# Kernel tuning notes

Measured on AMD Instinct MI355X. Metric: run time of the kernel, lower is better.

## Reference

```python
import jax, jax.numpy as jnp
import numpy as np

N_NODES = 100000
N_EDGES = 1600000
IN_F, HID_F, N_CLS = 512, 128, 64


def spmm(row, col, val, x, n):
    # out[i] = sum_{e: row[e]==i} val[e] * x[col[e]]  (sparse adj @ x)
    msgs = val[:, None] * x[col]          # [E, F] gather + scale
    return jax.ops.segment_sum(msgs, row, num_segments=n)


def setup_inputs() -> dict:
    key = jax.random.key(0)
    k = jax.random.split(key, 8)
    x = jax.random.normal(k[0], (N_NODES, IN_F), dtype=jnp.float32)
    adj_row = jax.random.randint(k[1], (N_EDGES,), 0, N_NODES, dtype=jnp.int32)
    adj_col = jax.random.randint(k[2], (N_EDGES,), 0, N_NODES, dtype=jnp.int32)
    adj_val = jax.random.uniform(k[3], (N_EDGES,), dtype=jnp.float32)
    s1 = 1.0 / np.sqrt(IN_F)
    s2 = 1.0 / np.sqrt(HID_F)
    w1 = jax.random.uniform(k[4], (IN_F, HID_F), jnp.float32, -s1, s1)
    b1 = jax.random.uniform(k[5], (HID_F,), jnp.float32, -s1, s1)
    w2 = jax.random.uniform(k[6], (HID_F, N_CLS), jnp.float32, -s2, s2)
    b2 = jax.random.uniform(k[7], (N_CLS,), jnp.float32, -s2, s2)
    return {"x": x, "adj_row": adj_row, "adj_col": adj_col, "adj_val": adj_val,
            "w1": w1, "b1": b1, "w2": w2, "b2": b2}


def reference(x, adj_row, adj_col, adj_val, w1, b1, w2, b2):
    n = x.shape[0]
    # conv1: dense projection then sparse aggregation
    h = spmm(adj_row, adj_col, adj_val, x @ w1 + b1, n)
    h = jax.nn.relu(h)  # dropout is identity in eval mode
    # conv2
    out = spmm(adj_row, adj_col, adj_val, h @ w2 + b2, n)
    return out
```

## Files before the change

### kernel.cpp

```cpp
#include <hip/hip_runtime.h>
#include <hip/hip_bf16.h>


constexpr int N_NODES = 100000;
constexpr int IN_F    = 512;
constexpr int HID_F   = 128;
constexpr int N_CLS   = 64;
constexpr int N_EDGES = 1600000;

constexpr int SCAN_BLOCK    = 256;
constexpr int N_SCAN_BLOCKS = (N_NODES + SCAN_BLOCK - 1) / SCAN_BLOCK;
constexpr int NB_GEMM       = (N_NODES + 255) / 256;

typedef __attribute__((ext_vector_type(8))) short short8;
typedef __attribute__((ext_vector_type(4))) float f32x4;

static __device__ __forceinline__ unsigned short f2bf(float x) {
    unsigned int u = __float_as_uint(x);
    unsigned int r = (u + 0x7FFFu + ((u >> 16) & 1u)) >> 16;
    return (unsigned short)r;
}
static __device__ __forceinline__ float bf2f(unsigned short u) {
    return __uint_as_float(((unsigned int)u) << 16);
}

__global__ void w1t_kernel(const float* __restrict__ w1, unsigned short* __restrict__ w1t)
{
    int idx = blockIdx.x * 256 + threadIdx.x;
    int n = idx >> 9, k = idx & 511;
    w1t[idx] = f2bf(w1[k * HID_F + n]);
}

__global__ void w2t_kernel(const float* __restrict__ w2, unsigned short* __restrict__ w2t)
{
    int idx = blockIdx.x * 256 + threadIdx.x;
    int n = idx >> 7, k = idx & 127;
    w2t[idx] = f2bf(w2[k * N_CLS + n]);
}

__global__ void zero_int_kernel(int* __restrict__ p, int n)
{
    int i = blockIdx.x * blockDim.x + threadIdx.x;
    if (i < n) p[i] = 0;
}

__global__ void hist_kernel(const int* __restrict__ row, int* __restrict__ counts)
{
    int e = blockIdx.x * blockDim.x + threadIdx.x;
    if (e < N_EDGES) atomicAdd(&counts[row[e]], 1);
}

__global__ __launch_bounds__(SCAN_BLOCK) void scanA_kernel(
    const int* __restrict__ counts, int* __restrict__ local_ex,
    int* __restrict__ blockSums)
{
    __shared__ int s[SCAN_BLOCK];
    const int t = threadIdx.x;
    const int i = blockIdx.x * SCAN_BLOCK + t;
    int v = (i < N_NODES) ? counts[i] : 0;
    s[t] = v;
    __syncthreads();
    for (int off = 1; off < SCAN_BLOCK; off <<= 1) {
        int u = (t >= off) ? s[t - off] : 0;
        __syncthreads();
        s[t] += u;
        __syncthreads();
    }
    if (i < N_NODES) local_ex[i] = s[t] - v;
    if (t == SCAN_BLOCK - 1) blockSums[blockIdx.x] = s[t];
}

__global__ __launch_bounds__(512) void scanB_kernel(int* __restrict__ blockSums)
{
    __shared__ int s[512];
    const int t = threadIdx.x;
    int v = (t < N_SCAN_BLOCKS) ? blockSums[t] : 0;
    s[t] = v;
    __syncthreads();
    for (int off = 1; off < 512; off <<= 1) {
        int u = (t >= off) ? s[t - off] : 0;
        __syncthreads();
        s[t] += u;
        __syncthreads();
    }
    if (t < N_SCAN_BLOCKS) blockSums[t] = s[t] - v;
}

__global__ __launch_bounds__(SCAN_BLOCK) void scanC_kernel(
    const int* __restrict__ local_ex, const int* __restrict__ blockSums,
    int* __restrict__ row_ptr, int* __restrict__ cursor)
{
    const int i = blockIdx.x * SCAN_BLOCK + threadIdx.x;
    if (i < N_NODES) {
        int v = local_ex[i] + blockSums[blockIdx.x];
        row_ptr[i] = v;
        cursor[i]  = v;
    }
    if (i == 0) row_ptr[N_NODES] = N_EDGES;
}

__global__ void scatter_kernel(
    const int* __restrict__ row, const int* __restrict__ col,
    const float* __restrict__ val, int* __restrict__ cursor,
    int2* __restrict__ es)
{
    int e = blockIdx.x * blockDim.x + threadIdx.x;
    if (e < N_EDGES) {
        int pos = atomicAdd(&cursor[row[e]], 1);
        es[pos] = make_int2(col[e], __float_as_int(val[e]));
    }
}

__global__ __launch_bounds__(512, 4) void gemm1_mfma_kernel(
    const float* __restrict__ x, const unsigned short* __restrict__ w1t,
    const float* __restrict__ b1, unsigned short* __restrict__ h0b)
{
    __shared__ unsigned short Bs[128 * 256];
    char* lb = (char*)Bs;

    const int tid  = threadIdx.x;
    const int lane = tid & 63;
    const int w    = tid >> 6;
    const int m = lane & 15;
    const int q = lane >> 4;
    const int row0 = blockIdx.x * 256 + w * 32;
    const bool active = row0 < N_NODES;

    f32x4 acc[2][8];
#pragma unroll
    for (int mi = 0; mi < 2; ++mi)
#pragma unroll
        for (int ni = 0; ni < 8; ++ni)
            acc[mi][ni] = (f32x4){0.f, 0.f, 0.f, 0.f};

    union U8 { short8 v; __hip_bfloat162 h[4]; };

    const float* a0p = x + (size_t)(row0 + m)      * IN_F + q * 8;
    const float* a1p = x + (size_t)(row0 + 16 + m) * IN_F + q * 8;
    const int swz = (m & 7) << 4;

    for (int p = 0; p < 2; ++p) {
        {
            const unsigned short* src = w1t + p * 256;
#pragma unroll
            for (int i = 0; i < 8; ++i) {
                int chunk = tid + i * 512;
                int n   = chunk >> 5;
                int k16 = chunk & 31;
                short8 v = *(const short8*)(src + (size_t)n * IN_F + k16 * 8);
                *(short8*)(lb + ((n * 512 + k16 * 16) ^ ((n & 7) << 4))) = v;
            }
        }
        __syncthreads();

        if (active) {
            const float* a0 = a0p + p * 256;
            const float* a1 = a1p + p * 256;
            float4 c0l = ((const float4*)a0)[0];
            float4 c0h = ((const float4*)a0)[1];
            float4 c1l = ((const float4*)a1)[0];
            float4 c1h = ((const float4*)a1)[1];

#pragma unroll
            for (int t = 0; t < 8; ++t) {
                float4 n0l, n0h, n1l, n1h;
                if (t + 1 < 8) {
                    n0l = ((const float4*)(a0 + (t + 1) * 32))[0];
                    n0h = ((const float4*)(a0 + (t + 1) * 32))[1];
                    n1l = ((const float4*)(a1 + (t + 1) * 32))[0];
                    n1h = ((const float4*)(a1 + (t + 1) * 32))[1];
                }

                U8 u0, u1;
                u0.h[0] = __float22bfloat162_rn(make_float2(c0l.x, c0l.y));
                u0.h[1] = __float22bfloat162_rn(make_float2(c0l.z, c0l.w));
                u0.h[2] = __float22bfloat162_rn(make_float2(c0h.x, c0h.y));
                u0.h[3] = __float22bfloat162_rn(make_float2(c0h.z, c0h.w));
                u1.h[0] = __float22bfloat162_rn(make_float2(c1l.x, c1l.y));
                u1.h[1] = __float22bfloat162_rn(make_float2(c1l.z, c1l.w));
                u1.h[2] = __float22bfloat162_rn(make_float2(c1h.x, c1h.y));
                u1.h[3] = __float22bfloat162_rn(make_float2(c1h.z, c1h.w));
                short8 av0 = u0.v, av1 = u1.v;

                const int kb = t * 64 + q * 16;
#pragma unroll
                for (int ni = 0; ni < 8; ++ni) {
                    int off = (((ni * 16 + m) * 512) + kb) ^ swz;
                    short8 bfr = *(const short8*)(lb + off);
                    acc[0][ni] = __builtin_amdgcn_mfma_f32_16x16x32_bf16(av0, bfr, acc[0][ni], 0, 0, 0);
                    acc[1][ni] = __builtin_amdgcn_mfma_f32_16x16x32_bf16(av1, bfr, acc[1][ni], 0, 0, 0);
                }

                c0l = n0l; c0h = n0h; c1l = n1l; c1h = n1h;
            }
        }
        __syncthreads();
    }

    if (!active) return;

    float bias[8];
#pragma unroll
    for (int ni = 0; ni < 8; ++ni) bias[ni] = b1[ni * 16 + m];

#pragma unroll
    for (int mi = 0; mi < 2; ++mi)
#pragma unroll
        for (int r = 0; r < 4; ++r) {
            int row = row0 + mi * 16 + q * 4 + r;
            unsigned short* dst = h0b + (size_t)row * HID_F;
#pragma unroll
            for (int ni = 0; ni < 8; ++ni)
                dst[ni * 16 + m] = f2bf(acc[mi][ni][r] + bias[ni]);
        }
}

__global__ __launch_bounds__(512, 4) void gemm2_mfma_kernel(
    const unsigned short* __restrict__ h1r, const unsigned short* __restrict__ w2t,
    const float* __restrict__ b2, float* __restrict__ h2)
{
    __shared__ unsigned short Bs[64 * 128];
    char* lb = (char*)Bs;

    const int tid  = threadIdx.x;
    const int lane = tid & 63;
    const int w    = tid >> 6;
    const int m = lane & 15;
    const int q = lane >> 4;
    const int row0 = blockIdx.x * 256 + w * 32;
    const bool active = row0 < N_NODES;

#pragma unroll
    for (int i = 0; i < 2; ++i) {
        int chunk = tid + i * 512;
        int n   = chunk >> 4;
        int k16 = chunk & 15;
        short8 v = *(const short8*)(w2t + (size_t)n * HID_F + k16 * 8);
        *(short8*)(lb + ((n * 256 + k16 * 16) ^ ((n & 7) << 4))) = v;
    }
    __syncthreads();
    if (!active) return;

    const unsigned short* a0p = h1r + (size_t)(row0 + m)      * HID_F + q * 8;
    const unsigned short* a1p = h1r + (size_t)(row0 + 16 + m) * HID_F + q * 8;

    short8 a0[4], a1[4];
#pragma unroll
    for (int t = 0; t < 4; ++t) {
        a0[t] = *(const short8*)(a0p + t * 32);
        a1[t] = *(const short8*)(a1p + t * 32);
    }

    f32x4 acc[2][4];
#pragma unroll
    for (int mi = 0; mi < 2; ++mi)
#pragma unroll
        for (int ni = 0; ni < 4; ++ni)
            acc[mi][ni] = (f32x4){0.f, 0.f, 0.f, 0.f};

    const int swz = (m & 7) << 4;
#pragma unroll
    for (int t = 0; t < 4; ++t) {
        const int kb = t * 64 + q * 16;
#pragma unroll
        for (int ni = 0; ni < 4; ++ni) {
            int off = (((ni * 16 + m) * 256) + kb) ^ swz;
            short8 b = *(const short8*)(lb + off);
            acc[0][ni] = __builtin_amdgcn_mfma_f32_16x16x32_bf16(a0[t], b, acc[0][ni], 0, 0, 0);
            acc[1][ni] = __builtin_amdgcn_mfma_f32_16x16x32_bf16(a1[t], b, acc[1][ni], 0, 0, 0);
        }
    }

    float bias[4];
#pragma unroll
    for (int ni = 0; ni < 4; ++ni) bias[ni] = b2[ni * 16 + m];

#pragma unroll
    for (int mi = 0; mi < 2; ++mi)
#pragma unroll
        for (int r = 0; r < 4; ++r) {
            int row = row0 + mi * 16 + q * 4 + r;
            float* dst = h2 + (size_t)row * N_CLS;
#pragma unroll
            for (int ni = 0; ni < 4; ++ni)
                dst[ni * 16 + m] = acc[mi][ni][r] + bias[ni];
        }
}

__global__ __launch_bounds__(256) void spmm_g128_kernel(
    const int* __restrict__ rp, const int2* __restrict__ es,
    const unsigned short* __restrict__ src, unsigned short* __restrict__ dst)
{
    const int r = blockIdx.x * 4 + threadIdx.y;
    if (r >= N_NODES) return;
    const int lane = threadIdx.x;
    const int j0 = rp[r], j1 = rp[r + 1];

    float ax = 0.f, ay = 0.f;
    int j = j0;
    for (; j + 7 < j1; j += 8) {
        int2 e[8];
        ushort2 u[8];
#pragma unroll
        for (int t = 0; t < 8; ++t) e[t] = es[j + t];
#pragma unroll
        for (int t = 0; t < 8; ++t)
            u[t] = ((const ushort2*)(src + (size_t)e[t].x * HID_F))[lane];
#pragma unroll
        for (int t = 0; t < 8; ++t) {
            float v = __int_as_float(e[t].y);
            ax += v * bf2f(u[t].x);
            ay += v * bf2f(u[t].y);
        }
    }
    if (j + 3 < j1) {
        int2 e[4];
        ushort2 u[4];
#pragma unroll
        for (int t = 0; t < 4; ++t) e[t] = es[j + t];
#pragma unroll
        for (int t = 0; t < 4; ++t)
            u[t] = ((const ushort2*)(src + (size_t)e[t].x * HID_F))[lane];
#pragma unroll
        for (int t = 0; t < 4; ++t) {
            float v = __int_as_float(e[t].y);
            ax += v * bf2f(u[t].x);
            ay += v * bf2f(u[t].y);
        }
        j += 4;
    }
    for (; j < j1; ++j) {
        int2 e = es[j];
        float v = __int_as_float(e.y);
        ushort2 u = ((const ushort2*)(src + (size_t)e.x * HID_F))[lane];
        ax += v * bf2f(u.x);
        ay += v * bf2f(u.y);
    }
    ushort2 o;
    o.x = f2bf(fmaxf(ax, 0.f));
    o.y = f2bf(fmaxf(ay, 0.f));
    ((ushort2*)(dst + (size_t)r * HID_F))[lane] = o;
}

__global__ __launch_bounds__(256) void spmm_g64_kernel(
    const int* __restrict__ rp, const int2* __restrict__ es,
    const float* __restrict__ src, float* __restrict__ dst)
{
    const int r = blockIdx.x * 4 + threadIdx.y;
    if (r >= N_NODES) return;
    const int lane = threadIdx.x;
    const int j0 = rp[r], j1 = rp[r + 1];

    float acc = 0.f;
    int j = j0;
    for (; j + 7 < j1; j += 8) {
        int2 e[8];
        float a[8];
#pragma unroll
        for (int t = 0; t < 8; ++t) e[t] = es[j + t];
#pragma unroll
        for (int t = 0; t < 8; ++t)
            a[t] = src[(size_t)e[t].x * N_CLS + lane];
#pragma unroll
        for (int t = 0; t < 8; ++t)
            acc += __int_as_float(e[t].y) * a[t];
    }
    if (j + 3 < j1) {
        int2 e[4];
        float a[4];
#pragma unroll
        for (int t = 0; t < 4; ++t) e[t] = es[j + t];
#pragma unroll
        for (int t = 0; t < 4; ++t)
            a[t] = src[(size_t)e[t].x * N_CLS + lane];
#pragma unroll
        for (int t = 0; t < 4; ++t)
            acc += __int_as_float(e[t].y) * a[t];
        j += 4;
    }
    for (; j < j1; ++j) {
        int2 e = es[j];
        acc += __int_as_float(e.y) * src[(size_t)e.x * N_CLS + lane];
    }
    dst[(size_t)r * N_CLS + lane] = acc;
}

extern "C" void kernel_launch(void* const* d_in, const int* in_sizes, int n_in,
                              void* d_out, int out_size, void* d_ws, size_t ws_size,
                              hipStream_t stream)
{
    const float* x       = (const float*)d_in[0];
    const int*   adj_row = (const int*)  d_in[1];
    const int*   adj_col = (const int*)  d_in[2];
    const float* adj_val = (const float*)d_in[3];
    const float* w1      = (const float*)d_in[4];
    const float* b1      = (const float*)d_in[5];
    const float* w2      = (const float*)d_in[6];
    const float* b2      = (const float*)d_in[7];
    float*       out     = (float*)d_out;

    char* ws = (char*)d_ws;
    unsigned short* h0b   = (unsigned short*)ws;
    unsigned short* h1r   = (unsigned short*)(ws + 25600000);
    float*          h2    = (float*)(ws + 51200000);
    int2*           es    = (int2*) (ws + 76800000);
    int*            rp    = (int*)  (ws + 89600000);
    int*            cur   = (int*)  (ws + 90000016);
    unsigned short* w1t   = (unsigned short*)(ws + 90400016);
    int*            lex   = (int*)  (ws + 90531088);
    int*            bsum  = (int*)  (ws + 90931088);
    unsigned short* w2t   = (unsigned short*)(ws + 90932656);

    w1t_kernel<<<IN_F * HID_F / 256, 256, 0, stream>>>(w1, w1t);
    w2t_kernel<<<HID_F * N_CLS / 256, 256, 0, stream>>>(w2, w2t);
    zero_int_kernel<<<(N_NODES + 255) / 256, 256, 0, stream>>>(cur, N_NODES);
    hist_kernel<<<(N_EDGES + 255) / 256, 256, 0, stream>>>(adj_row, cur);
    scanA_kernel<<<N_SCAN_BLOCKS, SCAN_BLOCK, 0, stream>>>(cur, lex, bsum);
    scanB_kernel<<<1, 512, 0, stream>>>(bsum);
    scanC_kernel<<<N_SCAN_BLOCKS, SCAN_BLOCK, 0, stream>>>(lex, bsum, rp, cur);
    scatter_kernel<<<(N_EDGES + 255) / 256, 256, 0, stream>>>(
        adj_row, adj_col, adj_val, cur, es);

    gemm1_mfma_kernel<<<NB_GEMM, 512, 0, stream>>>(x, w1t, b1, h0b);
    spmm_g128_kernel<<<(N_NODES + 3) / 4, dim3(64, 4), 0, stream>>>(
        rp, es, h0b, h1r);

    gemm2_mfma_kernel<<<NB_GEMM, 512, 0, stream>>>(h1r, w2t, b2, h2);
    spmm_g64_kernel<<<(N_NODES + 3) / 4, dim3(64, 4), 0, stream>>>(
        rp, es, h2, out);
}
```

Before: 660.1 us.

## Fuse GEMM1 with edge scatter and merge weight-prep and histogram kernels

The weight transpose, weight conversion and edge histogram kernels are merged into one prep kernel, and the zeroing kernel becomes a memset. GEMM1 is retiled to 64 rows per 256-thread block and interleaved with the CSR scatter in a single launch, with even blocks doing GEMM and odd blocks doing scatter. The aim is to overlap the atomic-bound scatter with the bandwidth-bound GEMM and to cut launch count. GEMM output is now staged through LDS so rows are written to global memory with coalesced 16-byte stores. The cost is reloading W1 tiles more often per row and mixing very different workloads in one grid.

```diff
diff --git a/kernel.cpp b/kernel.cpp
--- a/kernel.cpp
+++ b/kernel.cpp
@@ -10,7 +10,11 @@
 
 constexpr int SCAN_BLOCK    = 256;
 constexpr int N_SCAN_BLOCKS = (N_NODES + SCAN_BLOCK - 1) / SCAN_BLOCK;
-constexpr int NB_GEMM       = (N_NODES + 255) / 256;
+constexpr int NB_GEMM2      = (N_NODES + 255) / 256;
+
+constexpr int NB_G1 = (N_NODES + 63) / 64;
+constexpr int NB_SC = (N_EDGES + 1023) / 1024;
+constexpr int NB_FUSED = NB_G1 + NB_SC;
 
 typedef __attribute__((ext_vector_type(8))) short short8;
 typedef __attribute__((ext_vector_type(4))) float f32x4;
@@ -24,30 +28,25 @@
     return __uint_as_float(((unsigned int)u) << 16);
 }
 
-__global__ void w1t_kernel(const float* __restrict__ w1, unsigned short* __restrict__ w1t)
-{
-    int idx = blockIdx.x * 256 + threadIdx.x;
-    int n = idx >> 9, k = idx & 511;
-    w1t[idx] = f2bf(w1[k * HID_F + n]);
-}
-
-__global__ void w2t_kernel(const float* __restrict__ w2, unsigned short* __restrict__ w2t)
-{
-    int idx = blockIdx.x * 256 + threadIdx.x;
-    int n = idx >> 7, k = idx & 127;
-    w2t[idx] = f2bf(w2[k * N_CLS + n]);
-}
-
-__global__ void zero_int_kernel(int* __restrict__ p, int n)
-{
-    int i = blockIdx.x * blockDim.x + threadIdx.x;
-    if (i < n) p[i] = 0;
-}
-
-__global__ void hist_kernel(const int* __restrict__ row, int* __restrict__ counts)
-{
-    int e = blockIdx.x * blockDim.x + threadIdx.x;
-    if (e < N_EDGES) atomicAdd(&counts[row[e]], 1);
+__global__ __launch_bounds__(256) void prep_kernel(
+    const float* __restrict__ w1, const float* __restrict__ w2,
+    const int* __restrict__ row,
+    unsigned short* __restrict__ w1t, unsigned short* __restrict__ w2t,
+    int* __restrict__ counts)
+{
+    const int bid = blockIdx.x;
+    if (bid < 256) {
+        int idx = bid * 256 + threadIdx.x;
+        int n = idx >> 9, k = idx & 511;
+        w1t[idx] = f2bf(w1[k * HID_F + n]);
+    } else if (bid < 288) {
+        int idx = (bid - 256) * 256 + threadIdx.x;
+        int n = idx >> 7, k = idx & 127;
+        w2t[idx] = f2bf(w2[k * N_CLS + n]);
+    } else {
+        int e = (bid - 288) * 256 + threadIdx.x;
+        if (e < N_EDGES) atomicAdd(&counts[row[e]], 1);
+    }
 }
 
 __global__ __launch_bounds__(SCAN_BLOCK) void scanA_kernel(
@@ -99,23 +98,127 @@
     if (i == 0) row_ptr[N_NODES] = N_EDGES;
 }
 
-__global__ void scatter_kernel(
+__global__ __launch_bounds__(256, 4) void fused_g1_scatter_kernel(
+    const float* __restrict__ x, const unsigned short* __restrict__ w1t,
+    const float* __restrict__ b1, unsigned short* __restrict__ h0b,
     const int* __restrict__ row, const int* __restrict__ col,
     const float* __restrict__ val, int* __restrict__ cursor,
     int2* __restrict__ es)
 {
-    int e = blockIdx.x * blockDim.x + threadIdx.x;
-    if (e < N_EDGES) {
-        int pos = atomicAdd(&cursor[row[e]], 1);
-        es[pos] = make_int2(col[e], __float_as_int(val[e]));
-    }
-}
-
-__global__ __launch_bounds__(512, 4) void gemm1_mfma_kernel(
-    const float* __restrict__ x, const unsigned short* __restrict__ w1t,
-    const float* __restrict__ b1, unsigned short* __restrict__ h0b)
-{
-    __shared__ unsigned short Bs[128 * 256];
+    __shared__ unsigned short Bs[128 * 128];
+    char* lb = (char*)Bs;
+    const int tid = threadIdx.x;
+    const int bid = blockIdx.x;
+
+    if (bid & 1) {
+        const int base = (bid >> 1) * 1024 + tid;
+#pragma unroll
+        for (int i = 0; i < 4; ++i) {
+            int e = base + i * 256;
+            if (e < N_EDGES) {
+                int r = row[e];
+                int pos = atomicAdd(&cursor[r], 1);
+                es[pos] = make_int2(col[e], __float_as_int(val[e]));
+            }
+        }
+        return;
+    }
+
+    const int gid  = bid >> 1;
+    const int lane = tid & 63;
+    const int w    = tid >> 6;
+    const int m = lane & 15;
+    const int q = lane >> 4;
+    const int row0 = gid * 64;
+    const int myrow = row0 + w * 16 + m;
+    const int arow  = (myrow < N_NODES) ? myrow : (N_NODES - 1);
+
+    f32x4 acc[8];
+#pragma unroll
+    for (int ni = 0; ni < 8; ++ni)
+        acc[ni] = (f32x4){0.f, 0.f, 0.f, 0.f};
+
+    union U8 { short8 v; __hip_bfloat162 h[4]; };
+
+    const float* ap = x + (size_t)arow * IN_F + q * 8;
+    const int swz = (m & 7) << 4;
+
+    float4 a0l = ((const float4*)ap)[0];
+    float4 a0h = ((const float4*)ap)[1];
+    float4 a1l = ((const float4*)(ap + 32))[0];
+    float4 a1h = ((const float4*)(ap + 32))[1];
+
+#pragma unroll
+    for (int t = 0; t < 16; ++t) {
+        if ((t & 3) == 0) {
+            if (t) __syncthreads();
+            const unsigned short* src = w1t + (t >> 2) * 128;
+#pragma unroll
+            for (int i = 0; i < 8; ++i) {
+                int c = tid + i * 256;
+                int n = c >> 4, k16 = c & 15;
+                short8 v = *(const short8*)(src + (size_t)n * IN_F + k16 * 8);
+                *(short8*)(lb + ((n * 256 + k16 * 16) ^ ((n & 7) << 4))) = v;
+            }
+            __syncthreads();
+        }
+
+        float4 nl, nh;
+        if (t + 2 < 16) {
+            nl = ((const float4*)(ap + (t + 2) * 32))[0];
+            nh = ((const float4*)(ap + (t + 2) * 32))[1];
+        }
+
+        U8 u;
+        u.h[0] = __float22bfloat162_rn(make_float2(a0l.x, a0l.y));
+        u.h[1] = __float22bfloat162_rn(make_float2(a0l.z, a0l.w));
+        u.h[2] = __float22bfloat162_rn(make_float2(a0h.x, a0h.y));
+        u.h[3] = __float22bfloat162_rn(make_float2(a0h.z, a0h.w));
+        short8 av = u.v;
+
+        const int kb = (t & 3) * 64 + q * 16;
+#pragma unroll
+        for (int ni = 0; ni < 8; ++ni) {
+            int off = (((ni * 16 + m) << 8) + kb) ^ swz;
+            short8 bfr = *(const short8*)(lb + off);
+            acc[ni] = __builtin_amdgcn_mfma_f32_16x16x32_bf16(av, bfr, acc[ni], 0, 0, 0);
+        }
+
+        a0l = a1l; a0h = a1h; a1l = nl; a1h = nh;
+    }
+
+    __syncthreads();
+    {
+        float bias[8];
+#pragma unroll
+        for (int ni = 0; ni < 8; ++ni) bias[ni] = b1[ni * 16 + m];
+
+        char* cb = lb + w * 4352;
+#pragma unroll
+        for (int ni = 0; ni < 8; ++ni)
+#pragma unroll
+            for (int r = 0; r < 4; ++r)
+                *(unsigned short*)(cb + (q * 4 + r) * 272 + (ni * 16 + m) * 2) =
+                    f2bf(acc[ni][r] + bias[ni]);
+    }
+    __syncthreads();
+#pragma unroll
+    for (int i = 0; i < 4; ++i) {
+        int c = tid + i * 256;
+        int lr = c >> 4, c16 = c & 15;
+        int grow = row0 + lr;
+        if (grow < N_NODES) {
+            short8 v = *(const short8*)(lb + (lr >> 4) * 4352 + (lr & 15) * 272 + c16 * 16);
+            *(short8*)(h0b + (size_t)grow * HID_F + c16 * 8) = v;
+        }
+    }
+}
+
+__global__ __launch_bounds__(512, 4) void gemm2_mfma_kernel(
+    const unsigned short* __restrict__ h1r, const unsigned short* __restrict__ w2t,
+    const float* __restrict__ b2, float* __restrict__ h2)
+{
+    __shared__ unsigned short Bs[64 * 128];
     char* lb = (char*)Bs;
 
     const int tid  = threadIdx.x;
@@ -126,110 +229,6 @@
     const int row0 = blockIdx.x * 256 + w * 32;
     const bool active = row0 < N_NODES;
 
-    f32x4 acc[2][8];
-#pragma unroll
-    for (int mi = 0; mi < 2; ++mi)
-#pragma unroll
-        for (int ni = 0; ni < 8; ++ni)
-            acc[mi][ni] = (f32x4){0.f, 0.f, 0.f, 0.f};
-
-    union U8 { short8 v; __hip_bfloat162 h[4]; };
-
-    const float* a0p = x + (size_t)(row0 + m)      * IN_F + q * 8;
-    const float* a1p = x + (size_t)(row0 + 16 + m) * IN_F + q * 8;
-    const int swz = (m & 7) << 4;
-
-    for (int p = 0; p < 2; ++p) {
-        {
-            const unsigned short* src = w1t + p * 256;
-#pragma unroll
-            for (int i = 0; i < 8; ++i) {
-                int chunk = tid + i * 512;
-                int n   = chunk >> 5;
-                int k16 = chunk & 31;
-                short8 v = *(const short8*)(src + (size_t)n * IN_F + k16 * 8);
-                *(short8*)(lb + ((n * 512 + k16 * 16) ^ ((n & 7) << 4))) = v;
-            }
-        }
-        __syncthreads();
-
-        if (active) {
-            const float* a0 = a0p + p * 256;
-            const float* a1 = a1p + p * 256;
-            float4 c0l = ((const float4*)a0)[0];
-            float4 c0h = ((const float4*)a0)[1];
-            float4 c1l = ((const float4*)a1)[0];
-            float4 c1h = ((const float4*)a1)[1];
-
-#pragma unroll
-            for (int t = 0; t < 8; ++t) {
-                float4 n0l, n0h, n1l, n1h;
-                if (t + 1 < 8) {
-                    n0l = ((const float4*)(a0 + (t + 1) * 32))[0];
-                    n0h = ((const float4*)(a0 + (t + 1) * 32))[1];
-                    n1l = ((const float4*)(a1 + (t + 1) * 32))[0];
-                    n1h = ((const float4*)(a1 + (t + 1) * 32))[1];
-                }
-
-                U8 u0, u1;
-                u0.h[0] = __float22bfloat162_rn(make_float2(c0l.x, c0l.y));
-                u0.h[1] = __float22bfloat162_rn(make_float2(c0l.z, c0l.w));
-                u0.h[2] = __float22bfloat162_rn(make_float2(c0h.x, c0h.y));
-                u0.h[3] = __float22bfloat162_rn(make_float2(c0h.z, c0h.w));
-                u1.h[0] = __float22bfloat162_rn(make_float2(c1l.x, c1l.y));
-                u1.h[1] = __float22bfloat162_rn(make_float2(c1l.z, c1l.w));
-                u1.h[2] = __float22bfloat162_rn(make_float2(c1h.x, c1h.y));
-                u1.h[3] = __float22bfloat162_rn(make_float2(c1h.z, c1h.w));
-                short8 av0 = u0.v, av1 = u1.v;
-
-                const int kb = t * 64 + q * 16;
-#pragma unroll
-                for (int ni = 0; ni < 8; ++ni) {
-                    int off = (((ni * 16 + m) * 512) + kb) ^ swz;
-                    short8 bfr = *(const short8*)(lb + off);
-                    acc[0][ni] = __builtin_amdgcn_mfma_f32_16x16x32_bf16(av0, bfr, acc[0][ni], 0, 0, 0);
-                    acc[1][ni] = __builtin_amdgcn_mfma_f32_16x16x32_bf16(av1, bfr, acc[1][ni], 0, 0, 0);
-                }
-
-                c0l = n0l; c0h = n0h; c1l = n1l; c1h = n1h;
-            }
-        }
-        __syncthreads();
-    }
-
-    if (!active) return;
-
-    float bias[8];
-#pragma unroll
-    for (int ni = 0; ni < 8; ++ni) bias[ni] = b1[ni * 16 + m];
-
-#pragma unroll
-    for (int mi = 0; mi < 2; ++mi)
-#pragma unroll
-        for (int r = 0; r < 4; ++r) {
-            int row = row0 + mi * 16 + q * 4 + r;
-            unsigned short* dst = h0b + (size_t)row * HID_F;
-#pragma unroll
-            for (int ni = 0; ni < 8; ++ni)
-                dst[ni * 16 + m] = f2bf(acc[mi][ni][r] + bias[ni]);
-        }
-}
-
-__global__ __launch_bounds__(512, 4) void gemm2_mfma_kernel(
-    const unsigned short* __restrict__ h1r, const unsigned short* __restrict__ w2t,
-    const float* __restrict__ b2, float* __restrict__ h2)
-{
-    __shared__ unsigned short Bs[64 * 128];
-    char* lb = (char*)Bs;
-
-    const int tid  = threadIdx.x;
-    const int lane = tid & 63;
-    const int w    = tid >> 6;
-    const int m = lane & 15;
-    const int q = lane >> 4;
-    const int row0 = blockIdx.x * 256 + w * 32;
-    const bool active = row0 < N_NODES;
-
 #pragma unroll
     for (int i = 0; i < 2; ++i) {
         int chunk = tid + i * 512;
@@ -264,7 +263,7 @@
         const int kb = t * 64 + q * 16;
 #pragma unroll
         for (int ni = 0; ni < 4; ++ni) {
-            int off = (((ni * 16 + m) * 256) + kb) ^ swz;
+            int off = (((ni * 16 + m) << 8) + kb) ^ swz;
             short8 b = *(const short8*)(lb + off);
             acc[0][ni] = __builtin_amdgcn_mfma_f32_16x16x32_bf16(a0[t], b, acc[0][ni], 0, 0, 0);
             acc[1][ni] = __builtin_amdgcn_mfma_f32_16x16x32_bf16(a1[t], b, acc[1][ni], 0, 0, 0);
@@ -411,21 +410,19 @@
     int*            bsum  = (int*)  (ws + 90931088);
     unsigned short* w2t   = (unsigned short*)(ws + 90932656);
 
-    w1t_kernel<<<IN_F * HID_F / 256, 256, 0, stream>>>(w1, w1t);
-    w2t_kernel<<<HID_F * N_CLS / 256, 256, 0, stream>>>(w2, w2t);
-    zero_int_kernel<<<(N_NODES + 255) / 256, 256, 0, stream>>>(cur, N_NODES);
-    hist_kernel<<<(N_EDGES + 255) / 256, 256, 0, stream>>>(adj_row, cur);
+    hipMemsetAsync(cur, 0, N_NODES * sizeof(int), stream);
+    prep_kernel<<<288 + (N_EDGES + 255) / 256, 256, 0, stream>>>(
+        w1, w2, adj_row, w1t, w2t, cur);
     scanA_kernel<<<N_SCAN_BLOCKS, SCAN_BLOCK, 0, stream>>>(cur, lex, bsum);
     scanB_kernel<<<1, 512, 0, stream>>>(bsum);
     scanC_kernel<<<N_SCAN_BLOCKS, SCAN_BLOCK, 0, stream>>>(lex, bsum, rp, cur);
-    scatter_kernel<<<(N_EDGES + 255) / 256, 256, 0, stream>>>(
-        adj_row, adj_col, adj_val, cur, es);
-
-    gemm1_mfma_kernel<<<NB_GEMM, 512, 0, stream>>>(x, w1t, b1, h0b);
+
+    fused_g1_scatter_kernel<<<NB_FUSED, 256, 0, stream>>>(
+        x, w1t, b1, h0b, adj_row, adj_col, adj_val, cur, es);
     spmm_g128_kernel<<<(N_NODES + 3) / 4, dim3(64, 4), 0, stream>>>(
         rp, es, h0b, h1r);
 
-    gemm2_mfma_kernel<<<NB_GEMM, 512, 0, stream>>>(h1r, w2t, b2, h2);
+    gemm2_mfma_kernel<<<NB_GEMM2, 512, 0, stream>>>(h1r, w2t, b2, h2);
     spmm_g64_kernel<<<(N_NODES + 3) / 4, dim3(64, 4), 0, stream>>>(
         rp, es, h2, out);
 }
```

Measured after the change: 563.2 us. 14.7% less time.
